# Optimization experiments

Measured on AMD Instinct MI355X. Metric: run time of the kernel, lower is better.

The kernel has to match this reference:

```python
import jax, jax.numpy as jnp
import numpy as np

B, D_IN, D_COMMON = 16384, 2048, 1024
HIDDEN, D_OUT = 4096, 1024
N_EXPERTS = 4


def setup_inputs() -> dict:
    key = jax.random.key(0)
    ks = jax.random.split(key, 12)
    s = 0.02
    return {
        "x": jax.random.normal(ks[0], (B, D_IN), dtype=jnp.float32),
        "k": jax.random.randint(ks[1], (B,), 0, N_EXPERTS, dtype=jnp.int32),
        # per-key alignment Linear(D_IN -> D_COMMON), stored [in, out]
        "W_exp": jax.random.normal(ks[2], (N_EXPERTS, D_IN, D_COMMON), dtype=jnp.float32) * s,
        "b_exp": jax.random.normal(ks[3], (N_EXPERTS, D_COMMON), dtype=jnp.float32) * s,
        # dense MLP: common -> 4096 -> 4096 -> 1024
        "W1": jax.random.normal(ks[4], (D_COMMON, HIDDEN), dtype=jnp.float32) * s,
        "b1": jax.random.normal(ks[5], (HIDDEN,), dtype=jnp.float32) * s,
        "W2": jax.random.normal(ks[6], (HIDDEN, HIDDEN), dtype=jnp.float32) * s,
        "b2": jax.random.normal(ks[7], (HIDDEN,), dtype=jnp.float32) * s,
        "W3": jax.random.normal(ks[8], (HIDDEN, D_OUT), dtype=jnp.float32) * s,
        "b3": jax.random.normal(ks[9], (D_OUT,), dtype=jnp.float32) * s,
    }


def reference(x, k, W_exp, b_exp, W1, b1, W2, b2, W3, b3):
    # Key-routed per-row Linear: row i goes through expert k[i].
    # Compute all expert projections, then select per-row (vectorized dispatch).
    xW = jnp.einsum('bd,edc->ebc', x, W_exp)              # [E, B, common]
    onehot = jax.nn.one_hot(k, N_EXPERTS, dtype=x.dtype)  # [B, E]
    aligned = jnp.einsum('be,ebc->bc', onehot, xW) + b_exp[k]  # [B, common]
    # dense MLP with ReLU activations
    h = jax.nn.relu(aligned @ W1 + b1)
    h = jax.nn.relu(h @ W2 + b2)
    return h @ W3 + b3
```

## Files before the change

kernel.cpp:

```cpp
#include <hip/hip_runtime.h>
#include <stdint.h>

#define DEV static __device__ __forceinline__

typedef unsigned short u16;
typedef float  f32x4 __attribute__((ext_vector_type(4)));
typedef short  s16x8 __attribute__((ext_vector_type(8)));
typedef u16    u16x4 __attribute__((ext_vector_type(4)));

#define VMCNT(n) asm volatile("s_waitcnt vmcnt(" #n ")" ::: "memory")
#define BAR() __builtin_amdgcn_s_barrier()
#define MFMA16(d, va, vb) d = __builtin_amdgcn_mfma_f32_16x16x32_bf16(va, vb, d, 0, 0, 0)

DEV u16 f2bf(float f) {
  uint32_t u = __float_as_uint(f);
  u += 0x7FFFu + ((u >> 16) & 1u);
  return (u16)(u >> 16);
}

DEV void async16(const void* g, void* l) {
  __builtin_amdgcn_global_load_lds(
      (const __attribute__((address_space(1))) void*)g,
      (__attribute__((address_space(3))) void*)l, 16, 0, 0);
}

__global__ void route_zero(int* c) {
  if (threadIdx.x < 8) c[threadIdx.x] = 0;
}
__global__ void route_count(const int* __restrict__ k, int* __restrict__ c, int B) {
  int i = blockIdx.x * blockDim.x + threadIdx.x;
  if (i < B) atomicAdd(&c[k[i]], 1);
}
__global__ void route_scan(int* c) {
  if (threadIdx.x == 0) {
    int s = 0;
    for (int e = 0; e < 4; ++e) { c[8 + e] = s; s += c[e]; }
  }
}
__global__ void route_scatter(const int* __restrict__ k, int* __restrict__ c,
                              int* __restrict__ perm, int B) {
  int i = blockIdx.x * blockDim.x + threadIdx.x;
  if (i < B) {
    int e = k[i];
    int pos = atomicAdd(&c[4 + e], 1);
    perm[c[8 + e] + pos] = i;
  }
}

__global__ void cvt_f32_bf16(const float* __restrict__ src, u16* __restrict__ dst, long n4) {
  long i = (long)blockIdx.x * blockDim.x + threadIdx.x;
  long stride = (long)gridDim.x * blockDim.x;
  for (; i < n4; i += stride) {
    f32x4 v = ((const f32x4*)src)[i];
    u16x4 o;
    o.x = f2bf(v.x); o.y = f2bf(v.y); o.z = f2bf(v.z); o.w = f2bf(v.w);
    ((u16x4*)dst)[i] = o;
  }
}

__global__ void transpose_w(const float* __restrict__ src, u16* __restrict__ dst,
                            int R, int C) {
  __shared__ float t[32][33];
  long base = (long)blockIdx.z * R * C;
  int c0 = blockIdx.x * 32, r0 = blockIdx.y * 32;
  int tx = threadIdx.x, ty = threadIdx.y;
#pragma unroll
  for (int i = 0; i < 32; i += 8)
    t[ty + i][tx] = src[base + (long)(r0 + ty + i) * C + c0 + tx];
  __syncthreads();
#pragma unroll
  for (int i = 0; i < 32; i += 8)
    dst[base + (long)(c0 + ty + i) * R + r0 + tx] = f2bf(t[tx][ty + i]);
}


DEV void stageA(const u16* __restrict__ A, long K, long bm, int k0, int g,
                u16* lds, int tid) {
#pragma unroll
  for (int j = 0; j < 2; ++j) {
    int i = j * 512 + tid;
    int row = ((i >> 9) << 7) | (g << 6) | ((i >> 3) & 63);
    int p = (i & 7) * 16;
    int ke = (p ^ ((row & 7) << 4)) >> 1;
    async16(A + (bm + row) * K + k0 + ke, lds + row * 64 + (i & 7) * 8);
  }
}

DEV void stageB(const u16* __restrict__ Bt, long K, long bn, int k0, int g,
                u16* lds, int tid) {
#pragma unroll
  for (int j = 0; j < 2; ++j) {
    int i = j * 512 + tid;
    int col = ((i >> 8) << 6) | (g << 5) | ((i >> 3) & 31);
    int p = (i & 7) * 16;
    int ke = (p ^ ((col & 7) << 4)) >> 1;
    async16(Bt + (bn + col) * K + k0 + ke, lds + col * 64 + (i & 7) * 8);
  }
}

DEV void stageAg(const u16* __restrict__ X, long K, int k0, int g,
                 const long* ar, u16* lds, int tid) {
#pragma unroll
  for (int j = 0; j < 2; ++j) {
    int i = j * 512 + tid;
    int row = (j << 7) | (g << 6) | ((i >> 3) & 63);
    int p = (i & 7) * 16;
    int ke = (p ^ ((row & 7) << 4)) >> 1;
    async16(X + ar[j] * K + k0 + ke, lds + row * 64 + (i & 7) * 8);
  }
}

DEV s16x8 ldfrag(const u16* lds, int row, int ks, int lk) {
  int b = (ks * 64 + lk * 16) ^ ((row & 7) << 4);
  return *(const s16x8*)((const char*)(lds + row * 64) + b);
}

#define KT4(Ac, Bc, S1, S2, S3, S4)                                            \
  {                                                                            \
    _Pragma("unroll") for (int m = 0; m < 4; ++m)                              \
      _Pragma("unroll") for (int ks = 0; ks < 2; ++ks)                         \
        aa[m][ks] = ldfrag(Ac, wr * 128 + m * 16 + lr, ks, lk);                \
    _Pragma("unroll") for (int n = 0; n < 2; ++n)                              \
      _Pragma("unroll") for (int ks = 0; ks < 2; ++ks)                         \
        blo[n][ks] = ldfrag(Bc, wc * 64 + n * 16 + lr, ks, lk);                \
    S1;                                                                        \
    BAR();                                                                     \
    __builtin_amdgcn_s_setprio(1);                                             \
    _Pragma("unroll") for (int m = 0; m < 4; ++m)                              \
      _Pragma("unroll") for (int n = 0; n < 2; ++n)                            \
        _Pragma("unroll") for (int ks = 0; ks < 2; ++ks)                       \
          MFMA16(acc[m][n], aa[m][ks], blo[n][ks]);                            \
    __builtin_amdgcn_s_setprio(0);                                             \
    _Pragma("unroll") for (int n = 0; n < 2; ++n)                              \
      _Pragma("unroll") for (int ks = 0; ks < 2; ++ks)                         \
        bhi[n][ks] = ldfrag(Bc, wc * 64 + (n + 2) * 16 + lr, ks, lk);          \
    S2;                                                                        \
    BAR();                                                                     \
    __builtin_amdgcn_s_setprio(1);                                             \
    _Pragma("unroll") for (int m = 0; m < 4; ++m)                              \
      _Pragma("unroll") for (int n = 0; n < 2; ++n)                            \
        _Pragma("unroll") for (int ks = 0; ks < 2; ++ks)                       \
          MFMA16(acc[m][n + 2], aa[m][ks], bhi[n][ks]);                        \
    __builtin_amdgcn_s_setprio(0);                                             \
    _Pragma("unroll") for (int m = 0; m < 4; ++m)                              \
      _Pragma("unroll") for (int ks = 0; ks < 2; ++ks)                         \
        aa[m][ks] = ldfrag(Ac, wr * 128 + (m + 4) * 16 + lr, ks, lk);          \
    S3;                                                                        \
    BAR();                                                                     \
    __builtin_amdgcn_s_setprio(1);                                             \
    _Pragma("unroll") for (int m = 0; m < 4; ++m)                              \
      _Pragma("unroll") for (int n = 0; n < 2; ++n)                            \
        _Pragma("unroll") for (int ks = 0; ks < 2; ++ks)                       \
          MFMA16(acc[m + 4][n], aa[m][ks], blo[n][ks]);                        \
    __builtin_amdgcn_s_setprio(0);                                             \
    S4;                                                                        \
    VMCNT(6);                                                                  \
    BAR();                                                                     \
    __builtin_amdgcn_s_setprio(1);                                             \
    _Pragma("unroll") for (int m = 0; m < 4; ++m)                              \
      _Pragma("unroll") for (int n = 0; n < 2; ++n)                            \
        _Pragma("unroll") for (int ks = 0; ks < 2; ++ks)                       \
          MFMA16(acc[m + 4][n + 2], aa[m][ks], bhi[n][ks]);                    \
    __builtin_amdgcn_s_setprio(0);                                             \
  }

template <int RELU, int OUTF32>
__global__ __launch_bounds__(512, 2) void gemm256p(
    const u16* __restrict__ A, const u16* __restrict__ Bt,
    const float* __restrict__ bias, void* __restrict__ Cout, int N, int K) {
  __shared__ u16 Al[2][256 * 64];
  __shared__ u16 Bl[2][256 * 64];
  const int tid = threadIdx.x;
  const int lane = tid & 63, wid = tid >> 6;
  const int wr = wid >> 2, wc = wid & 3;
  const int lr = lane & 15, lk = lane >> 4;

  const int nby = N >> 8;
  const int nwg = gridDim.x;
  int wg = blockIdx.x;
  if ((nwg & 7) == 0) {
    const int q = nwg >> 3;
    wg = (wg & 7) * q + (wg >> 3);
  }
  const long bm = (long)(wg / nby) << 8;
  const long bn = (long)(wg % nby) << 8;

  const int nt = K >> 6;
  f32x4 acc[8][4] = {};
  s16x8 aa[4][2], blo[2][2], bhi[2][2];

  stageA(A, K, bm, 0, 0, Al[0], tid);
  stageB(Bt, K, bn, 0, 0, Bl[0], tid);
  stageB(Bt, K, bn, 0, 1, Bl[0], tid);
  stageA(A, K, bm, 0, 1, Al[0], tid);
  stageA(A, K, bm, 64, 0, Al[1], tid);
  stageB(Bt, K, bn, 64, 0, Bl[1], tid);
  stageB(Bt, K, bn, 64, 1, Bl[1], tid);
  VMCNT(6);
  BAR();

  const int ni = nt >> 1;
  for (int i2 = 0; i2 < ni; ++i2) {
    const int t0 = 2 * i2;
    const int kn1 = (t0 + 1) << 6;
    const int kn2 = ((t0 + 2 < nt) ? t0 + 2 : t0) << 6;
    const int kn3 = ((t0 + 3 < nt) ? t0 + 3 : t0 + 1) << 6;
    KT4(Al[0], Bl[0],
        stageA(A, K, bm, kn1, 1, Al[1], tid),
        stageA(A, K, bm, kn2, 0, Al[0], tid),
        stageB(Bt, K, bn, kn2, 0, Bl[0], tid),
        stageB(Bt, K, bn, kn2, 1, Bl[0], tid));
    KT4(Al[1], Bl[1],
        stageA(A, K, bm, kn2, 1, Al[0], tid),
        stageA(A, K, bm, kn3, 0, Al[1], tid),
        stageB(Bt, K, bn, kn3, 0, Bl[1], tid),
        stageB(Bt, K, bn, kn3, 1, Bl[1], tid));
  }

#pragma unroll
  for (int m = 0; m < 8; ++m) {
    const long r0 = bm + wr * 128 + m * 16 + lk * 4;
#pragma unroll
    for (int n = 0; n < 4; ++n) {
      const long col = bn + wc * 64 + n * 16 + lr;
      const float bv = bias[col];
#pragma unroll
      for (int j = 0; j < 4; ++j) {
        float v = acc[m][n][j] + bv;
        if (RELU) v = fmaxf(v, 0.0f);
        if (OUTF32) ((float*)Cout)[(r0 + j) * (long)N + col] = v;
        else        ((u16*)Cout)[(r0 + j) * (long)N + col] = f2bf(v);
      }
    }
  }
}

__global__ __launch_bounds__(512, 2) void gemm256e(
    const u16* __restrict__ X, const u16* __restrict__ Wt,
    const float* __restrict__ bexp, u16* __restrict__ Out,
    const int* __restrict__ perm, const int* __restrict__ cvec,
    int K, int N, int TPE) {
  __shared__ u16 Al[2][256 * 64];
  __shared__ u16 Bl[2][256 * 64];
  const int e = blockIdx.x / TPE;
  const int tile = blockIdx.x - e * TPE;
  const int cnt = cvec[e];
  if (tile * 256 >= cnt) return;
  const int start = cvec[8 + e];

  const int tid = threadIdx.x;
  const int lane = tid & 63, wid = tid >> 6;
  const int wr = wid >> 2, wc = wid & 3;
  const int lr = lane & 15, lk = lane >> 4;
  const long bn = (long)blockIdx.y << 8;
  const long wbase = (long)e * N;

  long ar[2][2];
#pragma unroll
  for (int g = 0; g < 2; ++g)
#pragma unroll
    for (int j = 0; j < 2; ++j) {
      int rie = tile * 256 + ((j << 7) | (g << 6) | ((tid >> 3) & 63));
      ar[g][j] = perm[start + (rie < cnt - 1 ? rie : cnt - 1)];
    }

  const int nt = K >> 6;
  f32x4 acc[8][4] = {};
  s16x8 aa[4][2], blo[2][2], bhi[2][2];

  stageAg(X, K, 0, 0, ar[0], Al[0], tid);
  stageB(Wt, K, wbase + bn, 0, 0, Bl[0], tid);
  stageB(Wt, K, wbase + bn, 0, 1, Bl[0], tid);
  stageAg(X, K, 0, 1, ar[1], Al[0], tid);
  stageAg(X, K, 64, 0, ar[0], Al[1], tid);
  stageB(Wt, K, wbase + bn, 64, 0, Bl[1], tid);
  stageB(Wt, K, wbase + bn, 64, 1, Bl[1], tid);
  VMCNT(6);
  BAR();

  const int ni = nt >> 1;
  for (int i2 = 0; i2 < ni; ++i2) {
    const int t0 = 2 * i2;
    const int kn1 = (t0 + 1) << 6;
    const int kn2 = ((t0 + 2 < nt) ? t0 + 2 : t0) << 6;
    const int kn3 = ((t0 + 3 < nt) ? t0 + 3 : t0 + 1) << 6;
    KT4(Al[0], Bl[0],
        stageAg(X, K, kn1, 1, ar[1], Al[1], tid),
        stageAg(X, K, kn2, 0, ar[0], Al[0], tid),
        stageB(Wt, K, wbase + bn, kn2, 0, Bl[0], tid),
        stageB(Wt, K, wbase + bn, kn2, 1, Bl[0], tid));
    KT4(Al[1], Bl[1],
        stageAg(X, K, kn2, 1, ar[1], Al[0], tid),
        stageAg(X, K, kn3, 0, ar[0], Al[1], tid),
        stageB(Wt, K, wbase + bn, kn3, 0, Bl[1], tid),
        stageB(Wt, K, wbase + bn, kn3, 1, Bl[1], tid));
  }

#pragma unroll
  for (int m = 0; m < 8; ++m) {
    const int rb = tile * 256 + wr * 128 + m * 16 + lk * 4;
#pragma unroll
    for (int j = 0; j < 4; ++j) {
      if (rb + j < cnt) {
        const long grow = perm[start + rb + j];
#pragma unroll
        for (int n = 0; n < 4; ++n) {
          const long col = bn + wc * 64 + n * 16 + lr;
          float v = acc[m][n][j] + bexp[wbase + col];
          Out[grow * (long)N + col] = f2bf(v);
        }
      }
    }
  }
}

extern "C" void kernel_launch(void* const* d_in, const int* in_sizes, int n_in,
                              void* d_out, int out_size, void* d_ws, size_t ws_size,
                              hipStream_t stream) {
  const float* x     = (const float*)d_in[0];
  const int*   kk    = (const int*)d_in[1];
  const float* W_exp = (const float*)d_in[2];
  const float* b_exp = (const float*)d_in[3];
  const float* W1    = (const float*)d_in[4];
  const float* b1    = (const float*)d_in[5];
  const float* W2    = (const float*)d_in[6];
  const float* b2    = (const float*)d_in[7];
  const float* W3    = (const float*)d_in[8];
  const float* b3    = (const float*)d_in[9];
  float* out = (float*)d_out;

  const int B = 16384, DIN = 2048, DC = 1024, H = 4096, DOUT = 1024, E = 4;

  uint8_t* ws = (uint8_t*)d_ws;
  const size_t MB = 1ull << 20;
  u16* xb    = (u16*)(ws + 0);
  u16* algn  = (u16*)(ws + 64 * MB);
  u16* h2    = (u16*)(ws + 0);
  u16* h1    = (u16*)(ws + 128 * MB);
  u16* wexpt = (u16*)(ws + 256 * MB);
  u16* w1t   = (u16*)(ws + 272 * MB);
  u16* w2t   = (u16*)(ws + 280 * MB);
  u16* w3t   = (u16*)(ws + 312 * MB);
  int* perm  = (int*)(ws + 320 * MB);
  int* cvec  = (int*)(ws + 320 * MB + 65536);

  route_zero<<<1, 64, 0, stream>>>(cvec);
  route_count<<<(B + 255) / 256, 256, 0, stream>>>(kk, cvec, B);
  route_scan<<<1, 64, 0, stream>>>(cvec);
  route_scatter<<<(B + 255) / 256, 256, 0, stream>>>(kk, cvec, perm, B);

  cvt_f32_bf16<<<2048, 256, 0, stream>>>(x, xb, (long)B * DIN / 4);
  dim3 tb(32, 8);
  transpose_w<<<dim3(DC / 32, DIN / 32, E), tb, 0, stream>>>(W_exp, wexpt, DIN, DC);
  transpose_w<<<dim3(H / 32, DC / 32, 1), tb, 0, stream>>>(W1, w1t, DC, H);
  transpose_w<<<dim3(H / 32, H / 32, 1), tb, 0, stream>>>(W2, w2t, H, H);
  transpose_w<<<dim3(DOUT / 32, H / 32, 1), tb, 0, stream>>>(W3, w3t, H, DOUT);

  const int TPE = B / 256;
  gemm256e<<<dim3(E * TPE, DC / 256), 512, 0, stream>>>(
      xb, wexpt, b_exp, algn, perm, cvec, DIN, DC, TPE);

  gemm256p<1, 0><<<dim3((B / 256) * (H / 256)), 512, 0, stream>>>(algn, w1t, b1, h1, H, DC);
  gemm256p<1, 0><<<dim3((B / 256) * (H / 256)), 512, 0, stream>>>(h1, w2t, b2, h2, H, H);
  gemm256p<0, 1><<<dim3((B / 256) * (DOUT / 256)), 512, 0, stream>>>(h2, w3t, b3, out, DOUT, H);
}
```

Before: 1.063 ms.

## Fuse routing into one kernel, widen transpose stores, drop a GEMM barrier

Replaces four routing launches (zero, count, scan, scatter) with a single one-block kernel that uses wave ballots and LDS atomics, cutting launch overhead. The weight transpose now handles 64-row tiles and writes packed bf16 pairs, giving wider stores. It also removes one barrier inside the GEMM main-loop macro, which shortens the sync chain but risks an LDS race if that barrier protected buffer reuse. A single-block router runs serially over all 16K keys, which could cost more than the launches it replaces.

```diff
diff --git a/kernel.cpp b/kernel.cpp
--- a/kernel.cpp
+++ b/kernel.cpp
@@ -24,27 +24,48 @@
       (__attribute__((address_space(3))) void*)l, 16, 0, 0);
 }
 
-__global__ void route_zero(int* c) {
-  if (threadIdx.x < 8) c[threadIdx.x] = 0;
-}
-__global__ void route_count(const int* __restrict__ k, int* __restrict__ c, int B) {
-  int i = blockIdx.x * blockDim.x + threadIdx.x;
-  if (i < B) atomicAdd(&c[k[i]], 1);
-}
-__global__ void route_scan(int* c) {
-  if (threadIdx.x == 0) {
+__global__ __launch_bounds__(1024) void route_all(const int* __restrict__ k,
+                                                  int* __restrict__ c,
+                                                  int* __restrict__ perm, int B) {
+  __shared__ int lc[12];
+  const int tid = threadIdx.x;
+  const int lane = tid & 63;
+  if (tid < 12) lc[tid] = 0;
+  __syncthreads();
+  for (int i = tid; i < B; i += 1024) {
+    int e = k[i];
+#pragma unroll
+    for (int v = 0; v < 4; ++v) {
+      unsigned long long m = __ballot(e == v);
+      if (m != 0ull && lane == __ffsll((long long)m) - 1)
+        atomicAdd(&lc[v], __popcll(m));
+    }
+  }
+  __syncthreads();
+  if (tid == 0) {
     int s = 0;
-    for (int e = 0; e < 4; ++e) { c[8 + e] = s; s += c[e]; }
-  }
-}
-__global__ void route_scatter(const int* __restrict__ k, int* __restrict__ c,
-                              int* __restrict__ perm, int B) {
-  int i = blockIdx.x * blockDim.x + threadIdx.x;
-  if (i < B) {
+    for (int e = 0; e < 4; ++e) { lc[8 + e] = s; s += lc[e]; }
+  }
+  __syncthreads();
+  for (int i = tid; i < B; i += 1024) {
     int e = k[i];
-    int pos = atomicAdd(&c[4 + e], 1);
-    perm[c[8 + e] + pos] = i;
-  }
+#pragma unroll
+    for (int v = 0; v < 4; ++v) {
+      unsigned long long m = __ballot(e == v);
+      if (m != 0ull) {
+        int leader = __ffsll((long long)m) - 1;
+        int base = 0;
+        if (lane == leader) base = atomicAdd(&lc[4 + v], __popcll(m));
+        base = __shfl(base, leader);
+        if (e == v) {
+          int rank = __popcll(m & ((1ull << lane) - 1ull));
+          perm[lc[8 + v] + base + rank] = i;
+        }
+      }
+    }
+  }
+  __syncthreads();
+  if (tid < 12) c[tid] = lc[tid];
 }
 
 __global__ void cvt_f32_bf16(const float* __restrict__ src, u16* __restrict__ dst, long n4) {
@@ -60,17 +81,22 @@
 
 __global__ void transpose_w(const float* __restrict__ src, u16* __restrict__ dst,
                             int R, int C) {
-  __shared__ float t[32][33];
+  __shared__ float t[64][33];
   long base = (long)blockIdx.z * R * C;
-  int c0 = blockIdx.x * 32, r0 = blockIdx.y * 32;
+  int c0 = blockIdx.x * 32, r0 = blockIdx.y * 64;
   int tx = threadIdx.x, ty = threadIdx.y;
 #pragma unroll
-  for (int i = 0; i < 32; i += 8)
+  for (int i = 0; i < 64; i += 8)
     t[ty + i][tx] = src[base + (long)(r0 + ty + i) * C + c0 + tx];
   __syncthreads();
 #pragma unroll
-  for (int i = 0; i < 32; i += 8)
-    dst[base + (long)(c0 + ty + i) * R + r0 + tx] = f2bf(t[tx][ty + i]);
+  for (int j = 0; j < 4; ++j) {
+    int cc = ty + 8 * j;
+    ushort2 v;
+    v.x = f2bf(t[2 * tx][cc]);
+    v.y = f2bf(t[2 * tx + 1][cc]);
+    *(ushort2*)&dst[base + (long)(c0 + cc) * R + r0 + 2 * tx] = v;
+  }
 }
 
 
@@ -146,7 +172,7 @@
       _Pragma("unroll") for (int ks = 0; ks < 2; ++ks)                         \
         aa[m][ks] = ldfrag(Ac, wr * 128 + (m + 4) * 16 + lr, ks, lk);          \
     S3;                                                                        \
-    BAR();                                                                     \
+                                   \
     __builtin_amdgcn_s_setprio(1);                                             \
     _Pragma("unroll") for (int m = 0; m < 4; ++m)                              \
       _Pragma("unroll") for (int n = 0; n < 2; ++n)                            \
@@ -344,17 +370,14 @@
   int* perm  = (int*)(ws + 320 * MB);
   int* cvec  = (int*)(ws + 320 * MB + 65536);
 
-  route_zero<<<1, 64, 0, stream>>>(cvec);
-  route_count<<<(B + 255) / 256, 256, 0, stream>>>(kk, cvec, B);
-  route_scan<<<1, 64, 0, stream>>>(cvec);
-  route_scatter<<<(B + 255) / 256, 256, 0, stream>>>(kk, cvec, perm, B);
+  route_all<<<1, 1024, 0, stream>>>(kk, cvec, perm, B);
 
   cvt_f32_bf16<<<2048, 256, 0, stream>>>(x, xb, (long)B * DIN / 4);
   dim3 tb(32, 8);
-  transpose_w<<<dim3(DC / 32, DIN / 32, E), tb, 0, stream>>>(W_exp, wexpt, DIN, DC);
-  transpose_w<<<dim3(H / 32, DC / 32, 1), tb, 0, stream>>>(W1, w1t, DC, H);
-  transpose_w<<<dim3(H / 32, H / 32, 1), tb, 0, stream>>>(W2, w2t, H, H);
-  transpose_w<<<dim3(DOUT / 32, H / 32, 1), tb, 0, stream>>>(W3, w3t, H, DOUT);
+  transpose_w<<<dim3(DC / 32, DIN / 64, E), tb, 0, stream>>>(W_exp, wexpt, DIN, DC);
+  transpose_w<<<dim3(H / 32, DC / 64, 1), tb, 0, stream>>>(W1, w1t, DC, H);
+  transpose_w<<<dim3(H / 32, H / 64, 1), tb, 0, stream>>>(W2, w2t, H, H);
+  transpose_w<<<dim3(DOUT / 32, H / 64, 1), tb, 0, stream>>>(W3, w3t, H, DOUT);
 
   const int TPE = B / 256;
   gemm256e<<<dim3(E * TPE, DC / 256), 512, 0, stream>>>(
```

Result: faster. 878.8 us (-17.3%).
